# Performance work log

Hardware: AMD Instinct MI355X
Metric: run time of the kernel (lower is better)

Reference implementation:

```python
import jax, jax.numpy as jnp
import numpy as np

SQ, SK, B, H, D = 2048, 2048, 2, 16, 64
LAYER_NUMBER = 1  # coeff for query_key_layer_scaling
MASK_FILL = -10000.0  # attention_mask_func fill value


def setup_inputs() -> dict:
    key = jax.random.key(0)
    kq, kk, kv = jax.random.split(key, 3)
    query_layer = jax.random.normal(kq, (SQ, B, H, D), dtype=jnp.float32)
    key_layer = jax.random.normal(kk, (SK, B, H, D), dtype=jnp.float32)
    value_layer = jax.random.normal(kv, (SK, B, H, D), dtype=jnp.float32)
    attention_mask = jnp.zeros((B, 1, SQ, SK), dtype=bool)  # ignored for causal mask type
    return {
        "query_layer": query_layer,
        "key_layer": key_layer,
        "value_layer": value_layer,
        "attention_mask": attention_mask,
    }


def reference(query_layer, key_layer, value_layer, attention_mask):
    sq, b, h, d = query_layer.shape
    sk = key_layer.shape[0]
    coeff = float(LAYER_NUMBER)
    norm_factor = np.sqrt(d) * coeff  # norm_factor = sqrt(d) * layer_number

    # BMM1: [b,h,sq,sk] scores, scaled by 1/norm_factor
    scores = jnp.einsum("sbhd,tbhd->bhst", query_layer, key_layer) / norm_factor

    # FusedScaleMaskSoftmax: scale by coeff in fp32, causal mask, softmax
    scores = scores.astype(jnp.float32) * coeff
    causal = jnp.triu(jnp.ones((sq, sk), dtype=bool), k=1)  # True above diagonal -> masked
    scores = jnp.where(causal[None, None], MASK_FILL, scores)
    probs = jax.nn.softmax(scores, axis=-1).astype(query_layer.dtype)

    # dropout p=0.0 -> identity

    # BMM2: context [sq,b,h,d] -> [sq,b,h*d]
    context = jnp.einsum("bhst,tbhd->sbhd", probs, value_layer)
    return context.reshape(sq, b, h * d)
```

## Files before the change

### kernel.cpp

```cpp
#include <hip/hip_runtime.h>

typedef short bf16x8 __attribute__((ext_vector_type(8)));
typedef float f32x4 __attribute__((ext_vector_type(4)));
typedef unsigned u32x4 __attribute__((ext_vector_type(4)));
typedef unsigned u32x2 __attribute__((ext_vector_type(2)));

#define RS 2048
#define LDSK 72
#define QSCALE 0.18033688011f

static __device__ __forceinline__ unsigned pkbf(float a, float b) {
    union { float f; unsigned u; } ua, ub; ua.f = a; ub.f = b;
    return ((ua.u + 0x8000u) >> 16) | ((ub.u + 0x8000u) & 0xffff0000u);
}

static __device__ __forceinline__ float fexp2(float x) { return exp2f(x); }

__global__ __launch_bounds__(256, 3)
void fa_fwd(const float* __restrict__ Q, const float* __restrict__ K,
            const float* __restrict__ V, float* __restrict__ Out)
{
    __shared__ short Ksh[2][64 * LDSK];
    __shared__ short Vt[2][64 * LDSK];
    __shared__ short Psh[4][16 * LDSK];

    const int qt = 31 - blockIdx.y;
    const int bh = blockIdx.x;
    const int base = bh * 64;
    const int tid = threadIdx.x;
    const int wave = tid >> 6, lane = tid & 63;
    const int n15 = lane & 15, quad = lane >> 4;
    const int q0 = qt * 64;

    const int krow = tid >> 2, kcg = (tid & 3) * 16;
    const int vkey = (tid & 31) * 2, vd = (tid >> 5) * 4;

    bf16x8 qf[2];
    {
        const float* qp = Q + (size_t)(q0 + wave * 16 + n15) * RS + base + quad * 8;
        #pragma unroll
        for (int ks = 0; ks < 2; ++ks) {
            f32x4 a0 = *(const f32x4*)(qp + ks * 32) * QSCALE;
            f32x4 a1 = *(const f32x4*)(qp + ks * 32 + 4) * QSCALE;
            union { u32x4 u; bf16x8 s; } w;
            w.u[0] = pkbf(a0[0], a0[1]); w.u[1] = pkbf(a0[2], a0[3]);
            w.u[2] = pkbf(a1[0], a1[1]); w.u[3] = pkbf(a1[2], a1[3]);
            qf[ks] = w.s;
        }
    }

    f32x4 O[4];
    #pragma unroll
    for (int i = 0; i < 4; ++i) O[i] = (f32x4){0.f, 0.f, 0.f, 0.f};
    float l = 0.f;

    f32x4 rk0, rk1, rk2, rk3, rv0, rv1, rv2, rv3;

    auto prefetch = [&](int kt) {
        const int kb = kt * 64;
        const float* kp = K + (size_t)(kb + krow) * RS + base + kcg;
        rk0 = *(const f32x4*)kp;       rk1 = *(const f32x4*)(kp + 4);
        rk2 = *(const f32x4*)(kp + 8); rk3 = *(const f32x4*)(kp + 12);
        const float* vp = V + (size_t)(kb + vkey) * RS + base + vd;
        rv0 = *(const f32x4*)vp;        rv1 = *(const f32x4*)(vp + RS);
        rv2 = *(const f32x4*)(vp + 32); rv3 = *(const f32x4*)(vp + RS + 32);
    };

    auto stage = [&](int buf) {
        u32x4 w0; w0[0] = pkbf(rk0[0], rk0[1]); w0[1] = pkbf(rk0[2], rk0[3]);
                  w0[2] = pkbf(rk1[0], rk1[1]); w0[3] = pkbf(rk1[2], rk1[3]);
        *(u32x4*)&Ksh[buf][krow * LDSK + kcg] = w0;
        u32x4 w1; w1[0] = pkbf(rk2[0], rk2[1]); w1[1] = pkbf(rk2[2], rk2[3]);
                  w1[2] = pkbf(rk3[0], rk3[1]); w1[3] = pkbf(rk3[2], rk3[3]);
        *(u32x4*)&Ksh[buf][krow * LDSK + kcg + 8] = w1;
        #pragma unroll
        for (int i = 0; i < 4; ++i) {
            *(unsigned*)&Vt[buf][(vd + i) * LDSK + vkey] = pkbf(rv0[i], rv1[i]);
            *(unsigned*)&Vt[buf][(vd + 32 + i) * LDSK + vkey] = pkbf(rv2[i], rv3[i]);
        }
    };

    auto compute = [&](int buf, int kb, bool diag) {
        f32x4 S[4];
        #pragma unroll
        for (int mb = 0; mb < 4; ++mb) {
            f32x4 s = (f32x4){0.f, 0.f, 0.f, 0.f};
            bf16x8 kf0 = *(const bf16x8*)&Ksh[buf][(mb * 16 + n15) * LDSK + quad * 8];
            s = __builtin_amdgcn_mfma_f32_16x16x32_bf16(kf0, qf[0], s, 0, 0, 0);
            bf16x8 kf1 = *(const bf16x8*)&Ksh[buf][(mb * 16 + n15) * LDSK + 32 + quad * 8];
            s = __builtin_amdgcn_mfma_f32_16x16x32_bf16(kf1, qf[1], s, 0, 0, 0);
            S[mb] = s;
        }
        if (diag) {
            int q = q0 + wave * 16 + n15;
            #pragma unroll
            for (int mb = 0; mb < 4; ++mb)
                #pragma unroll
                for (int r = 0; r < 4; ++r)
                    if (kb + mb * 16 + quad * 4 + r > q) S[mb][r] = -1e30f;
        }
        float rs = 0.f;
        #pragma unroll
        for (int mb = 0; mb < 4; ++mb) {
            float p0 = fexp2(S[mb][0]), p1 = fexp2(S[mb][1]);
            float p2 = fexp2(S[mb][2]), p3 = fexp2(S[mb][3]);
            rs += (p0 + p1) + (p2 + p3);
            u32x2 w; w[0] = pkbf(p0, p1); w[1] = pkbf(p2, p3);
            *(u32x2*)&Psh[wave][n15 * LDSK + mb * 16 + quad * 4] = w;
        }
        rs += __shfl_xor(rs, 16);
        rs += __shfl_xor(rs, 32);
        l += rs;
        bf16x8 pf0 = *(const bf16x8*)&Psh[wave][n15 * LDSK + quad * 8];
        bf16x8 pf1 = *(const bf16x8*)&Psh[wave][n15 * LDSK + 32 + quad * 8];
        #pragma unroll
        for (int db = 0; db < 4; ++db) {
            bf16x8 vf0 = *(const bf16x8*)&Vt[buf][(db * 16 + n15) * LDSK + quad * 8];
            O[db] = __builtin_amdgcn_mfma_f32_16x16x32_bf16(pf0, vf0, O[db], 0, 0, 0);
            bf16x8 vf1 = *(const bf16x8*)&Vt[buf][(db * 16 + n15) * LDSK + 32 + quad * 8];
            O[db] = __builtin_amdgcn_mfma_f32_16x16x32_bf16(pf1, vf1, O[db], 0, 0, 0);
        }
    };

    prefetch(0);
    stage(0);
    __syncthreads();
    for (int kt = 0; kt <= qt; ++kt) {
        const int cur = kt & 1;
        if (kt < qt) prefetch(kt + 1);
        compute(cur, kt * 64, kt == qt);
        if (kt < qt) stage(1 - cur);
        __syncthreads();
    }

    #pragma unroll
    for (int r = 0; r < 4; ++r) {
        float inv = 1.0f / __shfl(l, quad * 4 + r);
        size_t row = (size_t)(q0 + wave * 16 + quad * 4 + r) * RS + base;
        #pragma unroll
        for (int db = 0; db < 4; ++db)
            Out[row + db * 16 + n15] = O[db][r] * inv;
    }
}

extern "C" void kernel_launch(void* const* d_in, const int* in_sizes, int n_in,
                              void* d_out, int out_size, void* d_ws, size_t ws_size,
                              hipStream_t stream) {
    const float* Q = (const float*)d_in[0];
    const float* K = (const float*)d_in[1];
    const float* V = (const float*)d_in[2];
    float* Out = (float*)d_out;
    dim3 grid(32, 32);
    fa_fwd<<<grid, dim3(256), 0, stream>>>(Q, K, V, Out);
}
```

Before: 160.4 us.

## Precast K/V to bf16 in workspace and reorder blocks for causal balance

Adds a prep kernel that converts K to bf16 and V to a transposed bf16 layout in the workspace once. The attention kernel then loads half as many bytes per tile and skips per-tile conversion and transposition. It also drops LDS double buffering for higher occupancy, interleaves long and short query tiles in the grid order, and uses the native exp2 builtin. The cost is an extra kernel launch and a write/read of a workspace copy, and the original kernel is kept as a fallback when the workspace is too small.

```diff
diff --git a/kernel.cpp b/kernel.cpp
--- a/kernel.cpp
+++ b/kernel.cpp
@@ -4,21 +4,192 @@
 typedef float f32x4 __attribute__((ext_vector_type(4)));
 typedef unsigned u32x4 __attribute__((ext_vector_type(4)));
 typedef unsigned u32x2 __attribute__((ext_vector_type(2)));
+typedef unsigned short ushort_t;
 
 #define RS 2048
 #define LDSK 72
 #define QSCALE 0.18033688011f
+#define BH_STRIDE (2048*64)
 
 static __device__ __forceinline__ unsigned pkbf(float a, float b) {
     union { float f; unsigned u; } ua, ub; ua.f = a; ub.f = b;
     return ((ua.u + 0x8000u) >> 16) | ((ub.u + 0x8000u) & 0xffff0000u);
 }
 
-static __device__ __forceinline__ float fexp2(float x) { return exp2f(x); }
+static __device__ __forceinline__ float fexp2(float x) {
+#if __has_builtin(__builtin_amdgcn_exp2f)
+    return __builtin_amdgcn_exp2f(x);
+#else
+    return exp2f(x);
+#endif
+}
+
+__global__ __launch_bounds__(256)
+void prep_bf16(const float* __restrict__ K, const float* __restrict__ V,
+               ushort_t* __restrict__ Kbf, ushort_t* __restrict__ Vtb)
+{
+    __shared__ short Tt[64 * LDSK];
+    const int kt = blockIdx.x, bh = blockIdx.y;
+    const int t = threadIdx.x;
+
+    {
+        const int key = t >> 2, cq = (t & 3) * 16;
+        const float* kp = K + (size_t)(kt * 64 + key) * RS + bh * 64 + cq;
+        f32x4 a0 = *(const f32x4*)kp,     a1 = *(const f32x4*)(kp + 4);
+        f32x4 a2 = *(const f32x4*)(kp + 8), a3 = *(const f32x4*)(kp + 12);
+        u32x4 w0, w1;
+        w0[0] = pkbf(a0[0], a0[1]); w0[1] = pkbf(a0[2], a0[3]);
+        w0[2] = pkbf(a1[0], a1[1]); w0[3] = pkbf(a1[2], a1[3]);
+        w1[0] = pkbf(a2[0], a2[1]); w1[1] = pkbf(a2[2], a2[3]);
+        w1[2] = pkbf(a3[0], a3[1]); w1[3] = pkbf(a3[2], a3[3]);
+        ushort_t* kout = Kbf + (size_t)bh * BH_STRIDE + (size_t)(kt * 64 + key) * 64 + cq;
+        *(u32x4*)kout = w0;
+        *(u32x4*)(kout + 8) = w1;
+    }
+    {
+        const int vkey = (t & 31) * 2, vd = (t >> 5) * 8;
+        const float* vp = V + (size_t)(kt * 64 + vkey) * RS + bh * 64 + vd;
+        f32x4 b0 = *(const f32x4*)vp,        b1 = *(const f32x4*)(vp + 4);
+        f32x4 c0 = *(const f32x4*)(vp + RS), c1 = *(const f32x4*)(vp + RS + 4);
+        #pragma unroll
+        for (int i = 0; i < 4; ++i) {
+            *(unsigned*)&Tt[(vd + i) * LDSK + vkey]     = pkbf(b0[i], c0[i]);
+            *(unsigned*)&Tt[(vd + 4 + i) * LDSK + vkey] = pkbf(b1[i], c1[i]);
+        }
+    }
+    __syncthreads();
+    {
+        const int d = t >> 2, kq = (t & 3) * 16;
+        ushort_t* vout = Vtb + (size_t)bh * BH_STRIDE + (size_t)d * RS + kt * 64 + kq;
+        u32x4 w0 = *(const u32x4*)&Tt[d * LDSK + kq];
+        u32x4 w1 = *(const u32x4*)&Tt[d * LDSK + kq + 8];
+        *(u32x4*)vout = w0;
+        *(u32x4*)(vout + 8) = w1;
+    }
+}
+
+__global__ __launch_bounds__(256, 4)
+void fa_fwd2(const float* __restrict__ Q, const ushort_t* __restrict__ Kbf,
+             const ushort_t* __restrict__ Vtb, float* __restrict__ Out)
+{
+    __shared__ short Ksh[64 * LDSK];
+    __shared__ short Vt[64 * LDSK];
+    __shared__ short Psh[4][16 * LDSK];
+
+    const int x = blockIdx.x;
+    const int chunk = x >> 8, idx = x & 255;
+    const int bh = idx & 31, s = idx >> 5;
+    const int qt = (chunk == 0) ? (31 - s) : (chunk == 1) ? (23 - s)
+                 : (chunk == 2) ? s : (8 + s);
+    const int base = bh * 64;
+    const int tid = threadIdx.x;
+    const int wave = tid >> 6, lane = tid & 63;
+    const int n15 = lane & 15, quad = lane >> 4;
+    const int q0 = qt * 64;
+
+    const int r0 = tid >> 3, cc = (tid & 7) * 8;
+    const ushort_t* kb = Kbf + (size_t)bh * BH_STRIDE + r0 * 64 + cc;
+    const ushort_t* vb = Vtb + (size_t)bh * BH_STRIDE + (size_t)r0 * RS + cc;
+
+    bf16x8 qf[2];
+    {
+        const float* qp = Q + (size_t)(q0 + wave * 16 + n15) * RS + base + quad * 8;
+        #pragma unroll
+        for (int ks = 0; ks < 2; ++ks) {
+            f32x4 a0 = *(const f32x4*)(qp + ks * 32) * QSCALE;
+            f32x4 a1 = *(const f32x4*)(qp + ks * 32 + 4) * QSCALE;
+            union { u32x4 u; bf16x8 s; } w;
+            w.u[0] = pkbf(a0[0], a0[1]); w.u[1] = pkbf(a0[2], a0[3]);
+            w.u[2] = pkbf(a1[0], a1[1]); w.u[3] = pkbf(a1[2], a1[3]);
+            qf[ks] = w.s;
+        }
+    }
+
+    f32x4 O[4];
+    #pragma unroll
+    for (int i = 0; i < 4; ++i) O[i] = (f32x4){0.f, 0.f, 0.f, 0.f};
+    float l = 0.f;
+
+    u32x4 pk0, pk1, pv0, pv1;
+    auto prefetch = [&](int kt) {
+        const ushort_t* kp = kb + (size_t)kt * 4096;
+        pk0 = *(const u32x4*)kp;
+        pk1 = *(const u32x4*)(kp + 32 * 64);
+        const ushort_t* vp = vb + kt * 64;
+        pv0 = *(const u32x4*)vp;
+        pv1 = *(const u32x4*)(vp + 32 * RS);
+    };
+    auto stage = [&]() {
+        *(u32x4*)&Ksh[r0 * LDSK + cc] = pk0;
+        *(u32x4*)&Ksh[(r0 + 32) * LDSK + cc] = pk1;
+        *(u32x4*)&Vt[r0 * LDSK + cc] = pv0;
+        *(u32x4*)&Vt[(r0 + 32) * LDSK + cc] = pv1;
+    };
+
+    auto compute = [&](int kb_, bool diag) {
+        f32x4 S[4];
+        #pragma unroll
+        for (int mb = 0; mb < 4; ++mb) {
+            f32x4 sv = (f32x4){0.f, 0.f, 0.f, 0.f};
+            bf16x8 kf0 = *(const bf16x8*)&Ksh[(mb * 16 + n15) * LDSK + quad * 8];
+            sv = __builtin_amdgcn_mfma_f32_16x16x32_bf16(kf0, qf[0], sv, 0, 0, 0);
+            bf16x8 kf1 = *(const bf16x8*)&Ksh[(mb * 16 + n15) * LDSK + 32 + quad * 8];
+            sv = __builtin_amdgcn_mfma_f32_16x16x32_bf16(kf1, qf[1], sv, 0, 0, 0);
+            S[mb] = sv;
+        }
+        if (diag) {
+            int q = q0 + wave * 16 + n15;
+            #pragma unroll
+            for (int mb = 0; mb < 4; ++mb)
+                #pragma unroll
+                for (int r = 0; r < 4; ++r)
+                    if (kb_ + mb * 16 + quad * 4 + r > q) S[mb][r] = -1e30f;
+        }
+        float rs = 0.f;
+        #pragma unroll
+        for (int mb = 0; mb < 4; ++mb) {
+            float p0 = fexp2(S[mb][0]), p1 = fexp2(S[mb][1]);
+            float p2 = fexp2(S[mb][2]), p3 = fexp2(S[mb][3]);
+            rs += (p0 + p1) + (p2 + p3);
+            u32x2 w; w[0] = pkbf(p0, p1); w[1] = pkbf(p2, p3);
+            *(u32x2*)&Psh[wave][n15 * LDSK + mb * 16 + quad * 4] = w;
+        }
+        rs += __shfl_xor(rs, 16);
+        rs += __shfl_xor(rs, 32);
+        l += rs;
+        bf16x8 pf0 = *(const bf16x8*)&Psh[wave][n15 * LDSK + quad * 8];
+        bf16x8 pf1 = *(const bf16x8*)&Psh[wave][n15 * LDSK + 32 + quad * 8];
+        #pragma unroll
+        for (int db = 0; db < 4; ++db) {
+            bf16x8 vf0 = *(const bf16x8*)&Vt[(db * 16 + n15) * LDSK + quad * 8];
+            O[db] = __builtin_amdgcn_mfma_f32_16x16x32_bf16(pf0, vf0, O[db], 0, 0, 0);
+            bf16x8 vf1 = *(const bf16x8*)&Vt[(db * 16 + n15) * LDSK + 32 + quad * 8];
+            O[db] = __builtin_amdgcn_mfma_f32_16x16x32_bf16(pf1, vf1, O[db], 0, 0, 0);
+        }
+    };
+
+    prefetch(0);
+    for (int kt = 0; kt <= qt; ++kt) {
+        __syncthreads();
+        stage();
+        __syncthreads();
+        if (kt < qt) prefetch(kt + 1);
+        compute(kt * 64, kt == qt);
+    }
+
+    #pragma unroll
+    for (int r = 0; r < 4; ++r) {
+        float inv = 1.0f / __shfl(l, quad * 4 + r);
+        size_t row = (size_t)(q0 + wave * 16 + quad * 4 + r) * RS + base;
+        #pragma unroll
+        for (int db = 0; db < 4; ++db)
+            Out[row + db * 16 + n15] = O[db][r] * inv;
+    }
+}
 
 __global__ __launch_bounds__(256, 3)
-void fa_fwd(const float* __restrict__ Q, const float* __restrict__ K,
-            const float* __restrict__ V, float* __restrict__ Out)
+void fa_fwd_fb(const float* __restrict__ Q, const float* __restrict__ K,
+               const float* __restrict__ V, float* __restrict__ Out)
 {
     __shared__ short Ksh[2][64 * LDSK];
     __shared__ short Vt[2][64 * LDSK];
@@ -31,7 +202,6 @@
     const int wave = tid >> 6, lane = tid & 63;
     const int n15 = lane & 15, quad = lane >> 4;
     const int q0 = qt * 64;
-
     const int krow = tid >> 2, kcg = (tid & 3) * 16;
     const int vkey = (tid & 31) * 2, vd = (tid >> 5) * 4;
 
@@ -48,14 +218,11 @@
             qf[ks] = w.s;
         }
     }
-
     f32x4 O[4];
     #pragma unroll
     for (int i = 0; i < 4; ++i) O[i] = (f32x4){0.f, 0.f, 0.f, 0.f};
     float l = 0.f;
-
     f32x4 rk0, rk1, rk2, rk3, rv0, rv1, rv2, rv3;
-
     auto prefetch = [&](int kt) {
         const int kb = kt * 64;
         const float* kp = K + (size_t)(kb + krow) * RS + base + kcg;
@@ -65,7 +232,6 @@
         rv0 = *(const f32x4*)vp;        rv1 = *(const f32x4*)(vp + RS);
         rv2 = *(const f32x4*)(vp + 32); rv3 = *(const f32x4*)(vp + RS + 32);
     };
-
     auto stage = [&](int buf) {
         u32x4 w0; w0[0] = pkbf(rk0[0], rk0[1]); w0[1] = pkbf(rk0[2], rk0[3]);
                   w0[2] = pkbf(rk1[0], rk1[1]); w0[3] = pkbf(rk1[2], rk1[3]);
@@ -79,17 +245,16 @@
             *(unsigned*)&Vt[buf][(vd + 32 + i) * LDSK + vkey] = pkbf(rv2[i], rv3[i]);
         }
     };
-
     auto compute = [&](int buf, int kb, bool diag) {
         f32x4 S[4];
         #pragma unroll
         for (int mb = 0; mb < 4; ++mb) {
-            f32x4 s = (f32x4){0.f, 0.f, 0.f, 0.f};
+            f32x4 sv = (f32x4){0.f, 0.f, 0.f, 0.f};
             bf16x8 kf0 = *(const bf16x8*)&Ksh[buf][(mb * 16 + n15) * LDSK + quad * 8];
-            s = __builtin_amdgcn_mfma_f32_16x16x32_bf16(kf0, qf[0], s, 0, 0, 0);
+            sv = __builtin_amdgcn_mfma_f32_16x16x32_bf16(kf0, qf[0], sv, 0, 0, 0);
             bf16x8 kf1 = *(const bf16x8*)&Ksh[buf][(mb * 16 + n15) * LDSK + 32 + quad * 8];
-            s = __builtin_amdgcn_mfma_f32_16x16x32_bf16(kf1, qf[1], s, 0, 0, 0);
-            S[mb] = s;
+            sv = __builtin_amdgcn_mfma_f32_16x16x32_bf16(kf1, qf[1], sv, 0, 0, 0);
+            S[mb] = sv;
         }
         if (diag) {
             int q = q0 + wave * 16 + n15;
@@ -121,7 +286,6 @@
             O[db] = __builtin_amdgcn_mfma_f32_16x16x32_bf16(pf1, vf1, O[db], 0, 0, 0);
         }
     };
-
     prefetch(0);
     stage(0);
     __syncthreads();
@@ -132,7 +296,6 @@
         if (kt < qt) stage(1 - cur);
         __syncthreads();
     }
-
     #pragma unroll
     for (int r = 0; r < 4; ++r) {
         float inv = 1.0f / __shfl(l, quad * 4 + r);
@@ -150,6 +313,13 @@
     const float* K = (const float*)d_in[1];
     const float* V = (const float*)d_in[2];
     float* Out = (float*)d_out;
-    dim3 grid(32, 32);
-    fa_fwd<<<grid, dim3(256), 0, stream>>>(Q, K, V, Out);
-}
+
+    if (ws_size >= (size_t)2 * 32 * BH_STRIDE * sizeof(ushort_t)) {
+        ushort_t* Kbf = (ushort_t*)d_ws;
+        ushort_t* Vtb = Kbf + (size_t)32 * BH_STRIDE;
+        prep_bf16<<<dim3(32, 32), dim3(256), 0, stream>>>(K, V, Kbf, Vtb);
+        fa_fwd2<<<dim3(1024), dim3(256), 0, stream>>>(Q, Kbf, Vtb, Out);
+    } else {
+        fa_fwd_fb<<<dim3(32, 32), dim3(256), 0, stream>>>(Q, K, V, Out);
+    }
+}
```

After: 139.0 us. -13.4%, faster.
